# Performance work log

Measured on AMD Instinct MI355X. Metric: run time of the kernel, lower is better.

Reference implementation:

```python
import jax, jax.numpy as jnp
import numpy as np

DIM = 384
NH = 12
HEAD = DIM // NH
WS = (7, 7, 7)
L = WS[0] * WS[1] * WS[2]          # 343 tokens per window
NW = 64                             # number of windows (mask.shape[0])
B = 1                               # batch per window group
N = B * NW                          # leading dim of x
TBL = (2 * WS[0] - 1) * (2 * WS[1] - 1) * (2 * WS[2] - 1)  # 2197
SCALE = HEAD ** -0.5


def _rel_index():
    # Standard Swin 3D relative position index, shape (L, L), values in [0, TBL)
    coords = np.stack(np.meshgrid(*[np.arange(w) for w in WS], indexing='ij')).reshape(3, -1)  # (3, L)
    rel = coords[:, :, None] - coords[:, None, :]                     # (3, L, L)
    rel = rel + (np.array(WS) - 1)[:, None, None]                     # shift to >= 0
    s1 = (2 * WS[1] - 1) * (2 * WS[2] - 1)
    s2 = (2 * WS[2] - 1)
    idx = rel[0] * s1 + rel[1] * s2 + rel[2]
    return jnp.asarray(idx, jnp.int32)


def setup_inputs() -> dict:
    key = jax.random.key(0)
    k_x, k_m, k_qkv, k_tbl, k_pw = jax.random.split(key, 5)
    x = jax.random.normal(k_x, (N, L, DIM), dtype=jnp.float32)
    mask = jax.random.bernoulli(k_m, 0.5, (NW, L, L))                 # bool, True = masked
    qkv_w = jax.random.normal(k_qkv, (DIM, 3 * DIM), dtype=jnp.float32) * 0.02
    table = jax.random.normal(k_tbl, (TBL, NH), dtype=jnp.float32) * 0.02
    proj_w = jax.random.normal(k_pw, (DIM, DIM), dtype=jnp.float32) * 0.02
    proj_b = jnp.zeros((DIM,), dtype=jnp.float32)
    rel_idx = _rel_index()
    return {"x": x, "qkv_w": qkv_w, "table": table, "proj_w": proj_w,
            "proj_b": proj_b, "mask": mask, "rel_idx": rel_idx}


def reference(x, qkv_w, table, proj_w, proj_b, mask, rel_idx):
    n, l, _ = x.shape
    # QKV projection (no bias, qkv_bias=False)
    qkv = (x @ qkv_w).reshape(n, l, 3, NH, HEAD).transpose(2, 0, 3, 1, 4)  # (3, n, nh, l, ch)
    q, k, v = qkv[0], qkv[1], qkv[2]
    attn = jnp.einsum('nhlc,nhmc->nhlm', q * SCALE, k)                 # (n, nh, l, l)
    # gather relative position bias: (L*L, nh) -> (nh, L, L)
    bias = table[rel_idx.reshape(-1)].reshape(l, l, NH).transpose(2, 0, 1)
    attn = attn + bias[None]
    # per-window boolean mask: attn viewed as (batch, nw, nh, l, l)
    attn = attn.reshape(-1, NW, NH, l, l)
    attn = jnp.where(mask[None, :, None], -jnp.inf, attn).reshape(n, NH, l, l)
    attn = jax.nn.softmax(attn, axis=-1)
    out = jnp.einsum('nhlm,nhmc->nhlc', attn, v)                       # (n, nh, l, ch)
    out = out.transpose(0, 2, 1, 3).reshape(n, l, DIM)
    return out @ proj_w + proj_b
```

## Files before the change

### kernel.cpp

```cpp
#include <hip/hip_runtime.h>


#define DIMD 384
#define NHH 12
#define HEADD 32
#define LL 343
#define NWW 64
#define NTOK (NWW * LL)
#define MPT 176
#define MP (MPT * 128)
#define LP 352
#define QT 22
#define KS 40
#define VTS 360
#define PSB 40
#define MW 12
#define CSS 136
#define SCALE_ 0.17677669529663687f
#define LOG2E_ 1.4426950408889634f
#define NEGBIG_ (-1.0e4f)

typedef _Float16 f16;
typedef _Float16 v8h __attribute__((ext_vector_type(8)));
typedef _Float16 v4h __attribute__((ext_vector_type(4)));
typedef float v4f __attribute__((ext_vector_type(4)));

__device__ __forceinline__ void async_cp16(const void* g, void* l) {
    __builtin_amdgcn_global_load_lds(
        (const __attribute__((address_space(1))) void*)g,
        (__attribute__((address_space(3))) void*)l, 16, 0, 0);
}

constexpr size_t HBUF = (size_t)NHH * MP * HEADD * 2;
constexpr size_t OFF_Q    = 0;
constexpr size_t OFF_K    = OFF_Q  + HBUF;
constexpr size_t OFF_V    = OFF_K  + HBUF;
constexpr size_t OFF_AO   = OFF_V  + HBUF;
constexpr size_t OFF_BT   = OFF_AO + (size_t)MP * DIMD * 2;
constexpr size_t OFF_WT   = OFF_BT + (size_t)NHH * LP * LP * 4;
constexpr size_t OFF_PWT  = OFF_WT + (size_t)3 * DIMD * DIMD * 2;
constexpr size_t OFF_MTB  = OFF_PWT + (size_t)DIMD * DIMD * 2;

constexpr int SMEM_ATTN = LP * KS * 2 + 32 * VTS * 2 + LP * MW * 4 + 8 * 16 * PSB * 2;

#define S0 (NTOK * DIMD / 4)
#define S1 (3 * DIMD * DIMD)
#define S2 (DIMD * DIMD)
#define S3 (NHH * LP * LP)
#define S4 (NWW * MW * LP)
#define SPREP (S0 + S1 + S2 + S3 + S4)

__global__ __launch_bounds__(256) void prep_all(
    const float* __restrict__ x, f16* __restrict__ xh,
    const float* __restrict__ qkv_w, f16* __restrict__ wt,
    const float* __restrict__ proj_w, f16* __restrict__ pwt,
    const float* __restrict__ table, const int* __restrict__ rel, float* __restrict__ btf,
    const int* __restrict__ mask, unsigned int* __restrict__ mtb) {
    int t = blockIdx.x * 256 + threadIdx.x;
    if (t < S0) {
        float4 v = *(const float4*)(x + (size_t)t * 4);
        v4h o; o[0] = (f16)v.x; o[1] = (f16)v.y; o[2] = (f16)v.z; o[3] = (f16)v.w;
        *(v4h*)(xh + (size_t)t * 4) = o;
    } else if (t < S0 + S1) {
        int e = t - S0;
        int n = e / DIMD, k = e % DIMD;
        wt[e] = (f16)qkv_w[(size_t)k * (3 * DIMD) + n];
    } else if (t < S0 + S1 + S2) {
        int e = t - S0 - S1;
        int n = e / DIMD, k = e % DIMD;
        pwt[e] = (f16)proj_w[(size_t)k * DIMD + n];
    } else if (t < S0 + S1 + S2 + S3) {
        int e = t - S0 - S1 - S2;
        int h = e / (LP * LP), rem = e % (LP * LP);
        int rq = rem / (LP * 4);
        int rem2 = rem % (LP * 4);
        int col = rem2 >> 2, e2 = rem2 & 3;
        int r = rq * 4 + e2;
        float v = NEGBIG_;
        if (col < LL && r < LL) v = table[(size_t)rel[r * LL + col] * NHH + h] * LOG2E_;
        btf[e] = v;
    } else if (t < SPREP) {
        int e = t - S0 - S1 - S2 - S3;
        int n = e / (MW * LP), rem = e % (MW * LP);
        int wg = rem / LP, col = rem % LP;
        unsigned int wd = 0;
        if (col < LL) {
            int rbase = wg * 32;
#pragma unroll 4
            for (int b = 0; b < 32; ++b) {
                int r = rbase + b;
                if (r < LL && mask[((size_t)n * LL + r) * LL + col]) wd |= (1u << b);
            }
        }
        mtb[((size_t)n * LP + col) * MW + wg] = wd;
    }
}

__global__ __launch_bounds__(256) void qkv_gemm(
    const f16* __restrict__ xh, const f16* __restrict__ wt,
    f16* __restrict__ qb, f16* __restrict__ kb, f16* __restrict__ vb) {
    __shared__ f16 ABs[8192];
    f16* As = ABs;
    f16* Bs = ABs + 4096;
    const int lin = blockIdx.x;
    const int m0 = ((lin / 72) * 8 + (lin & 7)) * 128;
    const int n0 = ((lin >> 3) % 9) * 128;
    const int tid = threadIdx.x;
    const int wave = tid >> 6, lane = tid & 63;
    const int quad = lane >> 4, l15 = lane & 15;
    const int wm = (wave >> 1) * 64, wn = (wave & 1) * 64;
    const int srow = (lane >> 2);
    const int scol = (lane & 3) * 8;
    const f16* ga0 = xh + (size_t)(m0 + wave * 32 + srow) * DIMD + scol;
    const f16* ga1 = xh + (size_t)(m0 + wave * 32 + 16 + srow) * DIMD + scol;
    const f16* gb0 = wt + (size_t)(n0 + wave * 32 + srow) * DIMD + scol;
    const f16* gb1 = wt + (size_t)(n0 + wave * 32 + 16 + srow) * DIMD + scol;
    f16* la0 = As + (wave * 2) * 512;
    f16* la1 = As + (wave * 2 + 1) * 512;
    f16* lb0 = Bs + (wave * 2) * 512;
    f16* lb1 = Bs + (wave * 2 + 1) * 512;
    v4f acc[4][4] = {};
    for (int k0 = 0; k0 < DIMD; k0 += 32) {
        async_cp16(ga0 + k0, la0);
        async_cp16(ga1 + k0, la1);
        async_cp16(gb0 + k0, lb0);
        async_cp16(gb1 + k0, lb1);
        __syncthreads();
        v8h a[4], b[4];
#pragma unroll
        for (int i = 0; i < 4; ++i) a[i] = *(const v8h*)(As + (wm + i * 16 + l15) * 32 + quad * 8);
#pragma unroll
        for (int j = 0; j < 4; ++j) b[j] = *(const v8h*)(Bs + (wn + j * 16 + l15) * 32 + quad * 8);
#pragma unroll
        for (int i = 0; i < 4; ++i)
#pragma unroll
            for (int j = 0; j < 4; ++j)
                acc[i][j] = __builtin_amdgcn_mfma_f32_16x16x32_f16(a[i], b[j], acc[i][j], 0, 0, 0);
        __syncthreads();
    }
    const int t = n0 / DIMD;
    f16* dst = (t == 0) ? qb : (t == 1) ? kb : vb;
    const float sc = (t == 0) ? (SCALE_ * LOG2E_) : 1.0f;
    const int nrel = n0 - t * DIMD;
    f16* Cs = ABs;
    const int rl0 = (wave >> 1) * 16 + quad * 4;
#pragma unroll
    for (int i = 0; i < 4; ++i) {
#pragma unroll
        for (int e = 0; e < 4; ++e)
#pragma unroll
            for (int j = 0; j < 4; ++j)
                Cs[(rl0 + e) * CSS + wn + j * 16 + l15] = (f16)(acc[i][j][e] * sc);
        __syncthreads();
#pragma unroll
        for (int c = 0; c < 2; ++c) {
            int idx = c * 256 + tid;
            int rl = idx >> 4, col8 = (idx & 15) * 8;
            int gm = m0 + ((rl < 16) ? (i * 16 + rl) : (48 + i * 16 + rl));
            if (gm < NTOK) {
                int col = nrel + col8;
                size_t off = (size_t)(col >> 5) * ((size_t)MP * HEADD)
                           + (col & 31) + (size_t)gm * HEADD;
                *(v8h*)(dst + off) = *(const v8h*)(Cs + rl * CSS + col8);
            }
        }
        __syncthreads();
    }
}

__global__ __launch_bounds__(512, 4) void attn_kernel(
    const f16* __restrict__ qb, const f16* __restrict__ kb, const f16* __restrict__ vb,
    const float* __restrict__ biasT, const unsigned int* __restrict__ mtb,
    f16* __restrict__ ao) {
    extern __shared__ char smem[];
    f16* Ks  = (f16*)smem;
    f16* Vts = Ks + LP * KS;
    unsigned int* mtbL = (unsigned int*)(Vts + 32 * VTS);
    f16* Ps  = (f16*)(mtbL + LP * MW);
    const int n = blockIdx.x, h = blockIdx.y;
    const int tid = threadIdx.x, wave = tid >> 6, lane = tid & 63;
    const int quad = lane >> 4, l15 = lane & 15;
    const size_t slice = ((size_t)h * MP + n * LL) * HEADD;
    const f16* qg = qb + slice;
    const f16* kg = kb + slice;
    const f16* vg = vb + slice;
    for (int i = tid; i < LL * 8; i += 512) {
        int row = i >> 3, c4 = i & 7;
        *(ushort4*)(Ks + row * KS + c4 * 4) = *(const ushort4*)(kg + i * 4);
    }
    for (int i = tid; i < (LP - LL) * 8; i += 512) {
        int row = LL + (i >> 3), c4 = i & 7;
        *(ushort4*)(Ks + row * KS + c4 * 4) = make_ushort4(0, 0, 0, 0);
    }
    for (int i = tid; i < LL * 8; i += 512) {
        int key = i >> 3, c4 = (i & 7) * 4;
        ushort4 vv = *(const ushort4*)(vg + key * HEADD + c4);
        f16* d = Vts + c4 * VTS + key;
        d[0] = *(const f16*)&vv.x; d[VTS] = *(const f16*)&vv.y;
        d[2 * VTS] = *(const f16*)&vv.z; d[3 * VTS] = *(const f16*)&vv.w;
    }
    for (int i = tid; i < 32 * (LP - LL); i += 512) {
        int ch = i / (LP - LL), key = LL + i % (LP - LL);
        Vts[ch * VTS + key] = (f16)0.f;
    }
    {
        const unsigned int* mg = mtb + (size_t)n * LP * MW;
        for (int i = tid; i < LP * MW; i += 512) mtbL[i] = mg[i];
    }
    __syncthreads();
    f16* Pw = Ps + wave * (16 * PSB);
    const float* bth = biasT + (size_t)h * LP * LP;
    const v8h ones = {(f16)1.f, (f16)1.f, (f16)1.f, (f16)1.f,
                      (f16)1.f, (f16)1.f, (f16)1.f, (f16)1.f};
    for (int qt = wave; qt < QT; qt += 8) {
        v8h af = *(const v8h*)(qg + (qt * 16 + l15) * HEADD + quad * 8);
        const int r0 = qt * 16 + quad * 4;
        const int rword = r0 >> 5, rsh = r0 & 31;
        const float* bq = bth + (size_t)(qt * 4 + quad) * (LP * 4);
        v4f o0 = {}, o1 = {}, o2 = {};
        v4f cinN[2];
        cinN[0] = *(const v4f*)(bq + (size_t)l15 * 4);
        cinN[1] = *(const v4f*)(bq + (size_t)(16 + l15) * 4);
#pragma unroll
        for (int ktp = 0; ktp < 11; ++ktp) {
            v4f cin[2] = {cinN[0], cinN[1]};
            if (ktp < 10) {
                cinN[0] = *(const v4f*)(bq + (size_t)((ktp * 2 + 2) * 16 + l15) * 4);
                cinN[1] = *(const v4f*)(bq + (size_t)((ktp * 2 + 3) * 16 + l15) * 4);
            }
            unsigned int mw[2]; v8h bf[2]; v4f s[2];
#pragma unroll
            for (int half = 0; half < 2; ++half) {
                const int col = (ktp * 2 + half) * 16 + l15;
                mw[half] = mtbL[col * MW + rword];
                bf[half] = *(const v8h*)(Ks + col * KS + quad * 8);
            }
#pragma unroll
            for (int half = 0; half < 2; ++half) {
                v4f c = cin[half];
#pragma unroll
                for (int e = 0; e < 4; ++e)
                    if ((mw[half] >> (rsh + e)) & 1u) c[e] = NEGBIG_;
                s[half] = __builtin_amdgcn_mfma_f32_16x16x32_f16(af, bf[half], c, 0, 0, 0);
            }
#pragma unroll
            for (int half = 0; half < 2; ++half)
#pragma unroll
                for (int e = 0; e < 4; ++e) {
                    float p = __builtin_amdgcn_exp2f(s[half][e]);
                    Pw[(quad * 4 + e) * PSB + half * 16 + l15] = (f16)p;
                }
            v8h a  = *(const v8h*)(Pw + l15 * PSB + quad * 8);
            v8h b0 = *(const v8h*)(Vts + l15 * VTS + ktp * 32 + quad * 8);
            v8h b1 = *(const v8h*)(Vts + (16 + l15) * VTS + ktp * 32 + quad * 8);
            o0 = __builtin_amdgcn_mfma_f32_16x16x32_f16(a, b0, o0, 0, 0, 0);
            o1 = __builtin_amdgcn_mfma_f32_16x16x32_f16(a, b1, o1, 0, 0, 0);
            o2 = __builtin_amdgcn_mfma_f32_16x16x32_f16(a, ones, o2, 0, 0, 0);
        }
#pragma unroll
        for (int e = 0; e < 4; ++e) {
            int r = r0 + e;
            if (r < LL) {
                float inv = 1.f / o2[e];
                f16* orow = ao + ((size_t)(n * LL + r)) * DIMD + h * HEADD;
                orow[l15] = (f16)(o0[e] * inv);
                orow[16 + l15] = (f16)(o1[e] * inv);
            }
        }
    }
}

__global__ __launch_bounds__(256) void proj_gemm(
    const f16* __restrict__ ao, const f16* __restrict__ pwt,
    const float* __restrict__ pb, float* __restrict__ out) {
    __shared__ f16 As[128 * 32];
    __shared__ f16 Bs[128 * 32];
    const int lin = blockIdx.x;
    const int m0 = ((lin / 24) * 8 + (lin & 7)) * 128;
    const int n0 = ((lin >> 3) % 3) * 128;
    const int tid = threadIdx.x;
    const int wave = tid >> 6, lane = tid & 63;
    const int quad = lane >> 4, l15 = lane & 15;
    const int wm = (wave >> 1) * 64, wn = (wave & 1) * 64;
    const int srow = (lane >> 2);
    const int scol = (lane & 3) * 8;
    const f16* ga0 = ao + (size_t)(m0 + wave * 32 + srow) * DIMD + scol;
    const f16* ga1 = ao + (size_t)(m0 + wave * 32 + 16 + srow) * DIMD + scol;
    const f16* gb0 = pwt + (size_t)(n0 + wave * 32 + srow) * DIMD + scol;
    const f16* gb1 = pwt + (size_t)(n0 + wave * 32 + 16 + srow) * DIMD + scol;
    f16* la0 = As + (wave * 2) * 512;
    f16* la1 = As + (wave * 2 + 1) * 512;
    f16* lb0 = Bs + (wave * 2) * 512;
    f16* lb1 = Bs + (wave * 2 + 1) * 512;
    v4f acc[4][4] = {};
    for (int k0 = 0; k0 < DIMD; k0 += 32) {
        async_cp16(ga0 + k0, la0);
        async_cp16(ga1 + k0, la1);
        async_cp16(gb0 + k0, lb0);
        async_cp16(gb1 + k0, lb1);
        __syncthreads();
        v8h a[4], b[4];
#pragma unroll
        for (int i = 0; i < 4; ++i) a[i] = *(const v8h*)(As + (wm + i * 16 + l15) * 32 + quad * 8);
#pragma unroll
        for (int j = 0; j < 4; ++j) b[j] = *(const v8h*)(Bs + (wn + j * 16 + l15) * 32 + quad * 8);
#pragma unroll
        for (int i = 0; i < 4; ++i)
#pragma unroll
            for (int j = 0; j < 4; ++j)
                acc[i][j] = __builtin_amdgcn_mfma_f32_16x16x32_f16(a[i], b[j], acc[i][j], 0, 0, 0);
        __syncthreads();
    }
#pragma unroll
    for (int i = 0; i < 4; ++i)
#pragma unroll
        for (int e = 0; e < 4; ++e) {
            int gm = m0 + wm + i * 16 + quad * 4 + e;
            if (gm < NTOK) {
#pragma unroll
                for (int j = 0; j < 4; ++j) {
                    int gn = n0 + wn + j * 16 + l15;
                    out[(size_t)gm * DIMD + gn] = acc[i][j][e] + pb[gn];
                }
            }
        }
}

extern "C" void kernel_launch(void* const* d_in, const int* in_sizes, int n_in,
                              void* d_out, int out_size, void* d_ws, size_t ws_size,
                              hipStream_t stream) {
    const float* x      = (const float*)d_in[0];
    const float* qkv_w  = (const float*)d_in[1];
    const float* table  = (const float*)d_in[2];
    const float* proj_w = (const float*)d_in[3];
    const float* proj_b = (const float*)d_in[4];
    const int* mask     = (const int*)d_in[5];
    const int* rel      = (const int*)d_in[6];
    float* out = (float*)d_out;
    char* ws = (char*)d_ws;

    f16* q    = (f16*)(ws + OFF_Q);
    f16* k    = (f16*)(ws + OFF_K);
    f16* v    = (f16*)(ws + OFF_V);
    f16* xh   = (f16*)(ws + OFF_AO);
    f16* ao   = (f16*)(ws + OFF_AO);
    float* bt = (float*)(ws + OFF_BT);
    f16* wt   = (f16*)(ws + OFF_WT);
    f16* pwt  = (f16*)(ws + OFF_PWT);
    unsigned int* mtb = (unsigned int*)(ws + OFF_MTB);

    hipFuncSetAttribute((const void*)attn_kernel,
                        hipFuncAttributeMaxDynamicSharedMemorySize, SMEM_ATTN);

    prep_all<<<(SPREP + 255) / 256, 256, 0, stream>>>(
        x, xh, qkv_w, wt, proj_w, pwt, table, rel, bt, mask, mtb);
    qkv_gemm<<<dim3(MPT * 9), 256, 0, stream>>>(xh, wt, q, k, v);
    attn_kernel<<<dim3(NWW, NHH), 512, SMEM_ATTN, stream>>>(q, k, v, bt, mtb, ao);
    proj_gemm<<<dim3(MPT * 3), 256, 0, stream>>>(ao, pwt, proj_b, out);
}
```

Baseline: 227.1 us.

## Transpose attention MFMA roles, swizzle LDS tiles, and read mask bits from registers

The attention kernel now computes S^T by swapping the MFMA operands, so each lane owns one query row. This lets the per-row mask words be loaded once into registers, and the bias table and mask bitmaps are re-laid out in prep to match. K, V^T and P tiles in LDS drop their padded strides and use XOR swizzles instead. This shrinks shared memory so more blocks fit per CU (launch bounds raised to 6), and the mask copy into LDS is removed. The grid is also flattened and remapped across XCDs, and P is written with packed f16 conversions and vector output stores. The risks are bank conflicts in the new swizzle pattern and higher register pressure from holding twelve mask words per lane.

```diff
diff --git a/kernel.cpp b/kernel.cpp
--- a/kernel.cpp
+++ b/kernel.cpp
@@ -11,9 +11,6 @@
 #define MP (MPT * 128)
 #define LP 352
 #define QT 22
-#define KS 40
-#define VTS 360
-#define PSB 40
 #define MW 12
 #define CSS 136
 #define SCALE_ 0.17677669529663687f
@@ -29,6 +26,10 @@
     __builtin_amdgcn_global_load_lds(
         (const __attribute__((address_space(1))) void*)g,
         (__attribute__((address_space(3))) void*)l, 16, 0, 0);
+}
+
+__device__ __forceinline__ unsigned int pk2(float a, float b) {
+    return __builtin_bit_cast(unsigned int, __builtin_amdgcn_cvt_pkrtz(a, b));
 }
 
 constexpr size_t HBUF = (size_t)NHH * MP * HEADD * 2;
@@ -41,7 +42,7 @@
 constexpr size_t OFF_PWT  = OFF_WT + (size_t)3 * DIMD * DIMD * 2;
 constexpr size_t OFF_MTB  = OFF_PWT + (size_t)DIMD * DIMD * 2;
 
-constexpr int SMEM_ATTN = LP * KS * 2 + 32 * VTS * 2 + LP * MW * 4 + 8 * 16 * PSB * 2;
+constexpr int SMEM_ATTN = (LP * 32 + 32 * LP + 8 * 16 * 32) * 2;
 
 #define S0 (NTOK * DIMD / 4)
 #define S1 (3 * DIMD * DIMD)
@@ -72,27 +73,27 @@
     } else if (t < S0 + S1 + S2 + S3) {
         int e = t - S0 - S1 - S2;
         int h = e / (LP * LP), rem = e % (LP * LP);
-        int rq = rem / (LP * 4);
+        int kq = rem / (LP * 4);
         int rem2 = rem % (LP * 4);
         int col = rem2 >> 2, e2 = rem2 & 3;
-        int r = rq * 4 + e2;
+        int key = kq * 4 + e2;
         float v = NEGBIG_;
-        if (col < LL && r < LL) v = table[(size_t)rel[r * LL + col] * NHH + h] * LOG2E_;
+        if (col < LL && key < LL) v = table[(size_t)rel[col * LL + key] * NHH + h] * LOG2E_;
         btf[e] = v;
     } else if (t < SPREP) {
         int e = t - S0 - S1 - S2 - S3;
         int n = e / (MW * LP), rem = e % (MW * LP);
-        int wg = rem / LP, col = rem % LP;
+        int q = rem / MW, kw = rem % MW;
         unsigned int wd = 0;
-        if (col < LL) {
-            int rbase = wg * 32;
+        if (q < LL && kw < 11) {
+            int kbase = kw * 32;
+            int kmax = LL - kbase; if (kmax > 32) kmax = 32;
+            const int* mrow = mask + ((size_t)n * LL + q) * LL + kbase;
 #pragma unroll 4
-            for (int b = 0; b < 32; ++b) {
-                int r = rbase + b;
-                if (r < LL && mask[((size_t)n * LL + r) * LL + col]) wd |= (1u << b);
-            }
-        }
-        mtb[((size_t)n * LP + col) * MW + wg] = wd;
+            for (int b = 0; b < kmax; ++b)
+                if (mrow[b]) wd |= (1u << b);
+        }
+        mtb[((size_t)n * LP + q) * MW + kw] = wd;
     }
 }
 
@@ -168,104 +169,105 @@
     }
 }
 
-__global__ __launch_bounds__(512, 4) void attn_kernel(
+__global__ __launch_bounds__(512, 6) void attn_kernel(
     const f16* __restrict__ qb, const f16* __restrict__ kb, const f16* __restrict__ vb,
     const float* __restrict__ biasT, const unsigned int* __restrict__ mtb,
     f16* __restrict__ ao) {
     extern __shared__ char smem[];
     f16* Ks  = (f16*)smem;
-    f16* Vts = Ks + LP * KS;
-    unsigned int* mtbL = (unsigned int*)(Vts + 32 * VTS);
-    f16* Ps  = (f16*)(mtbL + LP * MW);
-    const int n = blockIdx.x, h = blockIdx.y;
+    f16* Vts = Ks + LP * 32;
+    f16* Ps  = Vts + 32 * LP;
+    const int bid = blockIdx.x;
+    const int j2 = (bid & 7) * 96 + (bid >> 3);
+    const int n = j2 & 63, h = j2 >> 6;
     const int tid = threadIdx.x, wave = tid >> 6, lane = tid & 63;
     const int quad = lane >> 4, l15 = lane & 15;
     const size_t slice = ((size_t)h * MP + n * LL) * HEADD;
     const f16* qg = qb + slice;
     const f16* kg = kb + slice;
     const f16* vg = vb + slice;
-    for (int i = tid; i < LL * 8; i += 512) {
-        int row = i >> 3, c4 = i & 7;
-        *(ushort4*)(Ks + row * KS + c4 * 4) = *(const ushort4*)(kg + i * 4);
-    }
-    for (int i = tid; i < (LP - LL) * 8; i += 512) {
-        int row = LL + (i >> 3), c4 = i & 7;
-        *(ushort4*)(Ks + row * KS + c4 * 4) = make_ushort4(0, 0, 0, 0);
-    }
-    for (int i = tid; i < LL * 8; i += 512) {
+    for (int i = tid; i < LP * 4; i += 512) {
+        int row = i >> 2, c8 = i & 3;
+        v8h vv = {};
+        if (row < LL) vv = *(const v8h*)(kg + (size_t)i * 8);
+        *(v8h*)(Ks + row * 32 + ((c8 ^ (row & 3)) << 3)) = vv;
+    }
+    for (int i = tid; i < LP * 8; i += 512) {
         int key = i >> 3, c4 = (i & 7) * 4;
-        ushort4 vv = *(const ushort4*)(vg + key * HEADD + c4);
-        f16* d = Vts + c4 * VTS + key;
-        d[0] = *(const f16*)&vv.x; d[VTS] = *(const f16*)&vv.y;
-        d[2 * VTS] = *(const f16*)&vv.z; d[3 * VTS] = *(const f16*)&vv.w;
-    }
-    for (int i = tid; i < 32 * (LP - LL); i += 512) {
-        int ch = i / (LP - LL), key = LL + i % (LP - LL);
-        Vts[ch * VTS + key] = (f16)0.f;
-    }
-    {
-        const unsigned int* mg = mtb + (size_t)n * LP * MW;
-        for (int i = tid; i < LP * MW; i += 512) mtbL[i] = mg[i];
+        ushort4 vv = make_ushort4(0, 0, 0, 0);
+        if (key < LL) vv = *(const ushort4*)(vg + (size_t)key * HEADD + c4);
+        int blk = key >> 3, off = key & 7;
+        Vts[(c4 + 0) * LP + ((blk ^ 0) << 3) + off] = *(const f16*)&vv.x;
+        Vts[(c4 + 1) * LP + ((blk ^ 1) << 3) + off] = *(const f16*)&vv.y;
+        Vts[(c4 + 2) * LP + ((blk ^ 2) << 3) + off] = *(const f16*)&vv.z;
+        Vts[(c4 + 3) * LP + ((blk ^ 3) << 3) + off] = *(const f16*)&vv.w;
     }
     __syncthreads();
-    f16* Pw = Ps + wave * (16 * PSB);
-    const float* bth = biasT + (size_t)h * LP * LP;
+    f16* Pw = Ps + wave * (16 * 32);
+    const float* bh = biasT + (size_t)h * LP * LP;
+    const unsigned int* mg = mtb + (size_t)n * LP * MW;
     const v8h ones = {(f16)1.f, (f16)1.f, (f16)1.f, (f16)1.f,
                       (f16)1.f, (f16)1.f, (f16)1.f, (f16)1.f};
+    const int pswz = (l15 >> 1) & 3;
+    const int kswz = (quad ^ (l15 & 3)) << 3;
     for (int qt = wave; qt < QT; qt += 8) {
-        v8h af = *(const v8h*)(qg + (qt * 16 + l15) * HEADD + quad * 8);
-        const int r0 = qt * 16 + quad * 4;
-        const int rword = r0 >> 5, rsh = r0 & 31;
-        const float* bq = bth + (size_t)(qt * 4 + quad) * (LP * 4);
+        const int q = qt * 16 + l15;
+        v8h af = *(const v8h*)(qg + (size_t)q * HEADD + quad * 8);
+        uint4 mA = *(const uint4*)(mg + q * MW);
+        uint4 mB = *(const uint4*)(mg + q * MW + 4);
+        uint4 mC = *(const uint4*)(mg + q * MW + 8);
+        unsigned int m[12] = {mA.x, mA.y, mA.z, mA.w, mB.x, mB.y, mB.z, mB.w,
+                              mC.x, mC.y, mC.z, mC.w};
+        const float* bq = bh + (size_t)q * 4;
+        v4f cinN[2];
+        cinN[0] = *(const v4f*)(bq + (size_t)(quad) * (LP * 4));
+        cinN[1] = *(const v4f*)(bq + (size_t)(4 + quad) * (LP * 4));
         v4f o0 = {}, o1 = {}, o2 = {};
-        v4f cinN[2];
-        cinN[0] = *(const v4f*)(bq + (size_t)l15 * 4);
-        cinN[1] = *(const v4f*)(bq + (size_t)(16 + l15) * 4);
 #pragma unroll
         for (int ktp = 0; ktp < 11; ++ktp) {
-            v4f cin[2] = {cinN[0], cinN[1]};
+            v4f cin0 = cinN[0], cin1 = cinN[1];
             if (ktp < 10) {
-                cinN[0] = *(const v4f*)(bq + (size_t)((ktp * 2 + 2) * 16 + l15) * 4);
-                cinN[1] = *(const v4f*)(bq + (size_t)((ktp * 2 + 3) * 16 + l15) * 4);
-            }
-            unsigned int mw[2]; v8h bf[2]; v4f s[2];
-#pragma unroll
-            for (int half = 0; half < 2; ++half) {
-                const int col = (ktp * 2 + half) * 16 + l15;
-                mw[half] = mtbL[col * MW + rword];
-                bf[half] = *(const v8h*)(Ks + col * KS + quad * 8);
-            }
-#pragma unroll
-            for (int half = 0; half < 2; ++half) {
-                v4f c = cin[half];
-#pragma unroll
-                for (int e = 0; e < 4; ++e)
-                    if ((mw[half] >> (rsh + e)) & 1u) c[e] = NEGBIG_;
-                s[half] = __builtin_amdgcn_mfma_f32_16x16x32_f16(af, bf[half], c, 0, 0, 0);
-            }
-#pragma unroll
-            for (int half = 0; half < 2; ++half)
-#pragma unroll
-                for (int e = 0; e < 4; ++e) {
-                    float p = __builtin_amdgcn_exp2f(s[half][e]);
-                    Pw[(quad * 4 + e) * PSB + half * 16 + l15] = (f16)p;
-                }
-            v8h a  = *(const v8h*)(Pw + l15 * PSB + quad * 8);
-            v8h b0 = *(const v8h*)(Vts + l15 * VTS + ktp * 32 + quad * 8);
-            v8h b1 = *(const v8h*)(Vts + (16 + l15) * VTS + ktp * 32 + quad * 8);
-            o0 = __builtin_amdgcn_mfma_f32_16x16x32_f16(a, b0, o0, 0, 0, 0);
-            o1 = __builtin_amdgcn_mfma_f32_16x16x32_f16(a, b1, o1, 0, 0, 0);
-            o2 = __builtin_amdgcn_mfma_f32_16x16x32_f16(a, ones, o2, 0, 0, 0);
-        }
-#pragma unroll
-        for (int e = 0; e < 4; ++e) {
-            int r = r0 + e;
-            if (r < LL) {
-                float inv = 1.f / o2[e];
-                f16* orow = ao + ((size_t)(n * LL + r)) * DIMD + h * HEADD;
-                orow[l15] = (f16)(o0[e] * inv);
-                orow[16 + l15] = (f16)(o1[e] * inv);
-            }
+                cinN[0] = *(const v4f*)(bq + (size_t)((ktp + 1) * 8 + quad) * (LP * 4));
+                cinN[1] = *(const v4f*)(bq + (size_t)((ktp + 1) * 8 + 4 + quad) * (LP * 4));
+            }
+            v8h bf0 = *(const v8h*)(Ks + (ktp * 32 + l15) * 32 + kswz);
+            v8h bf1 = *(const v8h*)(Ks + (ktp * 32 + 16 + l15) * 32 + kswz);
+            unsigned int mw = m[ktp];
+            unsigned int mb0 = mw >> (quad * 4);
+            unsigned int mb1 = mw >> (quad * 4 + 16);
+#pragma unroll
+            for (int e = 0; e < 4; ++e) {
+                if ((mb0 >> e) & 1u) cin0[e] = NEGBIG_;
+                if ((mb1 >> e) & 1u) cin1[e] = NEGBIG_;
+            }
+            v4f s0 = __builtin_amdgcn_mfma_f32_16x16x32_f16(bf0, af, cin0, 0, 0, 0);
+            v4f s1 = __builtin_amdgcn_mfma_f32_16x16x32_f16(bf1, af, cin1, 0, 0, 0);
+            unsigned int u0 = pk2(__builtin_amdgcn_exp2f(s0[0]), __builtin_amdgcn_exp2f(s0[1]));
+            unsigned int u1 = pk2(__builtin_amdgcn_exp2f(s0[2]), __builtin_amdgcn_exp2f(s0[3]));
+            unsigned int u2 = pk2(__builtin_amdgcn_exp2f(s1[0]), __builtin_amdgcn_exp2f(s1[1]));
+            unsigned int u3 = pk2(__builtin_amdgcn_exp2f(s1[2]), __builtin_amdgcn_exp2f(s1[3]));
+            f16* pr = Pw + l15 * 32 + (quad & 1) * 4;
+            *(uint2*)(pr + ((((quad >> 1) + 0) ^ pswz) << 3)) = make_uint2(u0, u1);
+            *(uint2*)(pr + ((((quad >> 1) + 2) ^ pswz) << 3)) = make_uint2(u2, u3);
+            v8h a = *(const v8h*)(Pw + l15 * 32 + ((quad ^ pswz) << 3));
+            int vblk = ((ktp * 4 + quad) ^ (l15 & 3)) << 3;
+            v8h w0 = *(const v8h*)(Vts + l15 * LP + vblk);
+            v8h w1 = *(const v8h*)(Vts + (16 + l15) * LP + vblk);
+            o0 = __builtin_amdgcn_mfma_f32_16x16x32_f16(w0, a, o0, 0, 0, 0);
+            o1 = __builtin_amdgcn_mfma_f32_16x16x32_f16(w1, a, o1, 0, 0, 0);
+            o2 = __builtin_amdgcn_mfma_f32_16x16x32_f16(ones, a, o2, 0, 0, 0);
+        }
+        if (q < LL) {
+            float inv = 1.0f / o2[0];
+            f16* orow = ao + ((size_t)(n * LL + q)) * DIMD + h * HEADD + quad * 4;
+            v4h w0, w1;
+#pragma unroll
+            for (int e = 0; e < 4; ++e) {
+                w0[e] = (f16)(o0[e] * inv);
+                w1[e] = (f16)(o1[e] * inv);
+            }
+            *(v4h*)(orow) = w0;
+            *(v4h*)(orow + 16) = w1;
         }
     }
 }
@@ -349,12 +351,12 @@
     f16* pwt  = (f16*)(ws + OFF_PWT);
     unsigned int* mtb = (unsigned int*)(ws + OFF_MTB);
 
-    hipFuncSetAttribute((const void*)attn_kernel,
-                        hipFuncAttributeMaxDynamicSharedMemorySize, SMEM_ATTN);
+    (void)hipFuncSetAttribute((const void*)attn_kernel,
+                              hipFuncAttributeMaxDynamicSharedMemorySize, SMEM_ATTN);
 
     prep_all<<<(SPREP + 255) / 256, 256, 0, stream>>>(
         x, xh, qkv_w, wt, proj_w, pwt, table, rel, bt, mask, mtb);
     qkv_gemm<<<dim3(MPT * 9), 256, 0, stream>>>(xh, wt, q, k, v);
-    attn_kernel<<<dim3(NWW, NHH), 512, SMEM_ATTN, stream>>>(q, k, v, bt, mtb, ao);
+    attn_kernel<<<dim3(NWW * NHH), 512, SMEM_ATTN, stream>>>(q, k, v, bt, mtb, ao);
     proj_gemm<<<dim3(MPT * 3), 256, 0, stream>>>(ao, pwt, proj_b, out);
 }
```

Measured after the change: 219.1 us. 1.04x faster.
